# Kernel tuning notes

Measured on AMD Instinct MI355X. Metric: run time of the kernel, lower is better.

## Reference

```python
import jax, jax.numpy as jnp
import numpy as np

T_PRED = 30   # max_pred_time * hz
B = 2048      # number of trajectory segments (batch)
D = 256       # n_hidden_after_deconv
DH = 128      # n_hidden_after_deconv / 2


def setup_inputs() -> dict:
    key = jax.random.key(0)
    k1, k2, k3, k4 = jax.random.split(key, 4)
    return {
        "encode_samples": jax.random.normal(k1, (T_PRED, B, D), dtype=jnp.float32),
        "representation_cur": jax.random.normal(k2, (B, DH), dtype=jnp.float32),
        "Wk_w": jax.random.normal(k3, (T_PRED, D, DH), dtype=jnp.float32) * (1.0 / np.sqrt(DH)),
        "Wk_b": jax.random.normal(k4, (T_PRED, D), dtype=jnp.float32) * 0.01,
    }


def reference(encode_samples, representation_cur, Wk_w, Wk_b):
    # encode_samples: [T, B, D] future encoder outputs (c_{t+i})
    # Wk_w: [T, D, DH] per-step Linear weights (torch layout [out,in]); Wk_b: [T, D]
    T, Bn, Dd = encode_samples.shape
    # pred[i] = Wk[i](representation_cur)  -> [T, B, D]
    pred = jnp.einsum('bh,tdh->tbd', representation_cur, Wk_w) + Wk_b[:, None, :]
    # total_i = encode_samples[i] @ pred[i].T  -> [T, B, B]
    totals = jnp.einsum('tbd,tcd->tbc', encode_samples, pred)
    # nce += sum(diag(log_softmax(total, dim=1))) per step (torch LogSoftmax default dim=1 on 2D)
    logp = jax.nn.log_softmax(totals, axis=2)
    nce = jnp.sum(jnp.diagonal(logp, axis1=1, axis2=2))
    calc_step = Bn * T  # all pred_steps > T-1 (all segments long enough)
    nce = nce / (-1.0 * calc_step)
    # accuracy from the LAST step (matches the original loop-carried `correct`/`batch_idx`)
    probs = jax.nn.softmax(totals[-1], axis=1)          # softmax over dim=1
    correct = jnp.sum(jnp.argmax(probs, axis=0) == jnp.arange(Bn))  # argmax over dim=0
    accuracy = correct.astype(jnp.float32) / Bn
    return (accuracy, nce, jnp.asarray(Bn), jnp.asarray(calc_step))
```

## Files before the change

### kernel.cpp

```cpp
#include <hip/hip_runtime.h>
#include <math.h>

typedef unsigned short u16;
typedef unsigned int   u32;
typedef unsigned long long u64;

#define T_PRED 30
#define BN 2048
#define DD 256
#define DHH 128
#define ESHIFT 64.0f

typedef __attribute__((ext_vector_type(8))) short short8;
typedef __attribute__((ext_vector_type(4))) float f32x4;

#define WS_S      4096
#define WS_TABLE  (WS_S + 245760)
#define WS_ZEND   (WS_TABLE + 16384)
#define WS_WH     WS_ZEND
#define WS_WL     (WS_WH + 1966080)
#define WS_RH     (WS_WL + 1966080)
#define WS_RL     (WS_RH + 524288)
#define WS_GH     (WS_RL + 524288)
#define WS_GL29   (WS_GH + 15728640)
#define WS_T29    (WS_GL29 + 524288)

__device__ __forceinline__ u16 bf16_rne(float f) {
    u32 u = __float_as_uint(f);
    u32 r = u + 0x7fffu + ((u >> 16) & 1u);
    return (u16)(r >> 16);
}

__device__ __forceinline__ short8 pack_hi8(const float* f) {
    short8 r;
#pragma unroll
    for (int k = 0; k < 8; ++k) r[k] = (short)(u16)(__float_as_uint(f[k]) >> 16);
    return r;
}
__device__ __forceinline__ short8 pack_lo8(const float* f) {
    short8 r;
#pragma unroll
    for (int k = 0; k < 8; ++k) {
        float hf = __uint_as_float(__float_as_uint(f[k]) & 0xffff0000u);
        r[k] = (short)bf16_rne(f[k] - hf);
    }
    return r;
}

#define AS1 __attribute__((address_space(1)))
#define AS3 __attribute__((address_space(3)))

__global__ __launch_bounds__(256) void prep_kernel(
    const float* __restrict__ rep, const float* __restrict__ Ww,
    u16* __restrict__ Rh, u16* __restrict__ Rl,
    u16* __restrict__ Wh, u16* __restrict__ Wl, u32* __restrict__ wsz)
{
    const int bx = blockIdx.x, tid = threadIdx.x;
    for (int i = bx * 256 + tid; i < 66560; i += 32768) wsz[i] = 0;

    if (bx < 120) {
        __shared__ float tile[64][132];
        const int t = bx >> 2, d0 = (bx & 3) * 64;
        for (int it = 0; it < 8; ++it) {
            int idx = tid + it * 256;
            int row = idx >> 5, off = (idx & 31) * 4;
            *(float4*)&tile[row][off] =
                *(const float4*)&Ww[((size_t)t * DD + d0 + row) * DHH + off];
        }
        __syncthreads();
        const int h = tid >> 1, half = tid & 1;
        const bool lo = (t == T_PRED - 1);
        for (int d4 = 0; d4 < 32; d4 += 4) {
            ushort4 hv, lv;
            u16* hp = (u16*)&hv; u16* lp = (u16*)&lv;
#pragma unroll
            for (int k = 0; k < 4; ++k) {
                float v = tile[half * 32 + d4 + k][h];
                u16 hb = bf16_rne(v);
                hp[k] = hb;
                float hf = __uint_as_float((u32)hb << 16);
                lp[k] = bf16_rne(v - hf);
            }
            size_t o = (size_t)t * DHH * DD + (size_t)h * DD + d0 + half * 32 + d4;
            *(ushort4*)&Wh[o] = hv;
            if (lo) *(ushort4*)&Wl[o] = lv;
        }
    } else {
        int base = (bx - 120) * 256 + tid;
        for (int p = 0; p < 32; ++p) {
            int i = base + p * 2048;
            float4 v = ((const float4*)rep)[i];
            float vv[4] = {v.x, v.y, v.z, v.w};
            u16 h[4], l[4];
#pragma unroll
            for (int k = 0; k < 4; ++k) {
                h[k] = bf16_rne(vv[k]);
                float hf = __uint_as_float((u32)h[k] << 16);
                l[k] = bf16_rne(vv[k] - hf);
            }
            ((ushort4*)Rh)[i] = make_ushort4(h[0], h[1], h[2], h[3]);
            ((ushort4*)Rl)[i] = make_ushort4(l[0], l[1], l[2], l[3]);
        }
    }
}

__global__ __launch_bounds__(256) void g_fused_kernel(
    const float* __restrict__ E, const u16* __restrict__ Wh,
    const u16* __restrict__ Wl, u16* __restrict__ Gh,
    u16* __restrict__ Gh29, u16* __restrict__ Gl29)
{
    __shared__ __attribute__((aligned(16))) u32 esm[2][4096];
    __shared__ __attribute__((aligned(16))) u16 wsm[2][4096];
    const int y    = blockIdx.y;
    const int tid  = threadIdx.x;
    const int lane = tid & 63;
    const int w    = tid >> 6;
    const int ml   = lane & 15;
    const int quad = lane >> 4;

    if (y < 29) {
        const int t    = y;
        const int row0 = blockIdx.x * 128;
        const int wr   = (w >> 1) * 64;
        const int wc   = (w & 1) * 64;
        const float* Et = E + (size_t)t * BN * DD;
        const u16*   Wt = Wh + (size_t)t * DHH * DD;
        const int erow_l = lane >> 3, eunit = lane & 7;
        const int wcol_l = lane >> 2, wunit = lane & 3;

        auto stage = [&](int buf, int kc) {
#pragma unroll
            for (int n = 0; n < 4; ++n) {
                int q = w * 4 + n;
                int row = q * 8 + erow_l;
                int unit = (eunit - row) & 7;
                const float* g = Et + (size_t)(row0 + row) * DD + kc * 32 + unit * 4;
                __builtin_amdgcn_global_load_lds((const AS1 u32*)g,
                    (AS3 u32*)(&esm[buf][q * 256]), 16, 0, 0);
            }
#pragma unroll
            for (int n = 0; n < 2; ++n) {
                int q = w * 2 + n;
                int col = q * 16 + wcol_l;
                int unit = (wunit - col) & 3;
                const u16* g = Wt + (size_t)col * DD + kc * 32 + unit * 8;
                __builtin_amdgcn_global_load_lds((const AS1 u32*)g,
                    (AS3 u32*)(&wsm[buf][q * 512]), 16, 0, 0);
            }
        };

        f32x4 acc[4][4];
#pragma unroll
        for (int i = 0; i < 4; ++i)
#pragma unroll
            for (int j = 0; j < 4; ++j) acc[i][j] = (f32x4){0.f, 0.f, 0.f, 0.f};

        stage(0, 0);
        __syncthreads();
#pragma unroll 1
        for (int kc = 0; kc < 8; ++kc) {
            if (kc < 7) stage((kc + 1) & 1, kc + 1);
            const int pb = kc & 1;
            short8 ah[4], bh[4];
#pragma unroll
            for (int i = 0; i < 4; ++i) {
                int row = wr + i * 16 + ml;
                float4 f0 = *(const float4*)&esm[pb][row * 32 + (((quad * 2 + 0 + row) & 7) * 4)];
                float4 f1 = *(const float4*)&esm[pb][row * 32 + (((quad * 2 + 1 + row) & 7) * 4)];
                float f[8] = {f0.x, f0.y, f0.z, f0.w, f1.x, f1.y, f1.z, f1.w};
                ah[i] = pack_hi8(f);
            }
#pragma unroll
            for (int j = 0; j < 4; ++j) {
                int col = wc + j * 16 + ml;
                bh[j] = *(const short8*)&wsm[pb][col * 32 + ((quad + col) & 3) * 8];
            }
#pragma unroll
            for (int i = 0; i < 4; ++i)
#pragma unroll
                for (int j = 0; j < 4; ++j)
                    acc[i][j] = __builtin_amdgcn_mfma_f32_16x16x32_bf16(ah[i], bh[j], acc[i][j], 0, 0, 0);
            __syncthreads();
        }

#pragma unroll
        for (int i = 0; i < 4; ++i)
#pragma unroll
            for (int j = 0; j < 4; ++j)
#pragma unroll
                for (int r = 0; r < 4; ++r) {
                    int row = row0 + wr + i * 16 + quad * 4 + r;
                    int col = wc + j * 16 + ml;
                    Gh[((size_t)t * BN + row) * DHH + col] = bf16_rne(acc[i][j][r]);
                }
    } else {
        const int row0 = ((y - 29) * 16 + blockIdx.x) * 32;
        const int wc   = w * 32;
        const size_t tE = (size_t)(T_PRED - 1) * BN * DD;
        const size_t tW = (size_t)(T_PRED - 1) * DHH * DD;

#pragma unroll 1
        for (int rr = 0; rr < 32; rr += 16) {
            f32x4 acc[2];
            acc[0] = (f32x4){0.f, 0.f, 0.f, 0.f};
            acc[1] = (f32x4){0.f, 0.f, 0.f, 0.f};
#pragma unroll
            for (int kc = 0; kc < 8; ++kc) {
                const float* ep = E + tE + (size_t)(row0 + rr + ml) * DD + kc * 32 + quad * 8;
                float4 e0 = *(const float4*)ep;
                float4 e1 = *(const float4*)(ep + 4);
                float f[8] = {e0.x, e0.y, e0.z, e0.w, e1.x, e1.y, e1.z, e1.w};
                short8 ah = pack_hi8(f);
                short8 al = pack_lo8(f);
#pragma unroll
                for (int j = 0; j < 2; ++j) {
                    size_t o = tW + (size_t)(wc + j * 16 + ml) * DD + kc * 32 + quad * 8;
                    short8 bh = *(const short8*)(Wh + o);
                    short8 bl = *(const short8*)(Wl + o);
                    acc[j] = __builtin_amdgcn_mfma_f32_16x16x32_bf16(ah, bh, acc[j], 0, 0, 0);
                    acc[j] = __builtin_amdgcn_mfma_f32_16x16x32_bf16(ah, bl, acc[j], 0, 0, 0);
                    acc[j] = __builtin_amdgcn_mfma_f32_16x16x32_bf16(al, bh, acc[j], 0, 0, 0);
                }
            }
#pragma unroll
            for (int j = 0; j < 2; ++j)
#pragma unroll
                for (int r = 0; r < 4; ++r) {
                    int row = row0 + rr + quad * 4 + r;
                    int col = wc + j * 16 + ml;
                    float v = acc[j][r];
                    u16 hb = bf16_rne(v);
                    float hf = __uint_as_float((u32)hb << 16);
                    Gh29[(size_t)row * DHH + col] = hb;
                    Gl29[(size_t)row * DHH + col] = bf16_rne(v - hf);
                }
        }
    }
}

__global__ __launch_bounds__(512, 4) void nce_fused_kernel(
    const u16* __restrict__ Gh, const u16* __restrict__ Gh29,
    const u16* __restrict__ Gl29, const u16* __restrict__ Rh,
    const u16* __restrict__ Rl, float* __restrict__ S,
    float* __restrict__ tot29, float* __restrict__ nce_acc)
{
    __shared__ __attribute__((aligned(16))) u16 sm[32768];
    const int z    = blockIdx.z;
    const int tid  = threadIdx.x;
    const int lane = tid & 63;
    const int w    = tid >> 6;
    const int ml   = lane & 15;
    const int quad = lane >> 4;
    float* S29 = S + (size_t)(T_PRED - 1) * BN;

    if (z < 29) {
        const int t  = z;
        const int c0 = (int)blockIdx.x << 8;
        const int r0 = (int)blockIdx.y << 8;

#pragma unroll
        for (int n = 0; n < 8; ++n) {
            const int q   = (w << 3) + n;
            const int U   = (q << 6) | lane;
            const int col = U >> 4;
            const int g   = ((U & 15) - col) & 15;
            const u16* src = Rh + (size_t)(c0 + col) * DHH + g * 8;
            __builtin_amdgcn_global_load_lds((const AS1 u32*)src,
                (AS3 u32*)(&sm[q << 9]), 16, 0, 0);
        }

        short8 ah[2][4];
#pragma unroll
        for (int i = 0; i < 2; ++i)
#pragma unroll
            for (int kc = 0; kc < 4; ++kc)
                ah[i][kc] = *(const short8*)(Gh +
                    ((size_t)t * BN + r0 + (w << 5) + (i << 4) + ml) * DHH
                    + (kc << 5) + (quad << 3));

        float ssum[2][4];
#pragma unroll
        for (int i = 0; i < 2; ++i)
#pragma unroll
            for (int r = 0; r < 4; ++r) ssum[i][r] = 0.f;
        float dsum = 0.f;
        const bool dblk = (c0 == r0);
        const int rbase = r0 + (w << 5) + (quad << 2);

        __syncthreads();

#pragma unroll 1
        for (int ch = 0; ch < 8; ++ch) {
            f32x4 acc[2][2];
#pragma unroll
            for (int i = 0; i < 2; ++i)
#pragma unroll
                for (int j = 0; j < 2; ++j) acc[i][j] = (f32x4){0.f, 0.f, 0.f, 0.f};

#pragma unroll
            for (int kc = 0; kc < 4; ++kc) {
                const int slot = ((kc << 2) + quad + ml) & 15;
                const short8 bh0 = *(const short8*)&sm[((ch << 5) + ml) * 128 + (slot << 3)];
                const short8 bh1 = *(const short8*)&sm[((ch << 5) + 16 + ml) * 128 + (slot << 3)];
                acc[0][0] = __builtin_amdgcn_mfma_f32_16x16x32_bf16(ah[0][kc], bh0, acc[0][0], 0, 0, 0);
                acc[0][1] = __builtin_amdgcn_mfma_f32_16x16x32_bf16(ah[0][kc], bh1, acc[0][1], 0, 0, 0);
                acc[1][0] = __builtin_amdgcn_mfma_f32_16x16x32_bf16(ah[1][kc], bh0, acc[1][0], 0, 0, 0);
                acc[1][1] = __builtin_amdgcn_mfma_f32_16x16x32_bf16(ah[1][kc], bh1, acc[1][1], 0, 0, 0);
            }

#pragma unroll
            for (int i = 0; i < 2; ++i)
#pragma unroll
                for (int j = 0; j < 2; ++j)
#pragma unroll
                    for (int r = 0; r < 4; ++r) {
                        float v = acc[i][j][r];
                        ssum[i][r] += __expf(v - ESHIFT);
                        if (dblk) {
                            int row = rbase + (i << 4) + r;
                            int col = c0 + (ch << 5) + (j << 4) + ml;
                            if (row == col) dsum += v;
                        }
                    }
        }

#pragma unroll
        for (int i = 0; i < 2; ++i)
#pragma unroll
            for (int r = 0; r < 4; ++r) {
                float v = ssum[i][r];
#pragma unroll
                for (int o = 1; o < 16; o <<= 1) v += __shfl_xor(v, o, 64);
                if (ml == 0)
                    atomicAdd(S + (size_t)t * BN + rbase + (i << 4) + r, v);
            }
        if (dblk) {
            float dv = dsum;
#pragma unroll
            for (int o = 1; o < 64; o <<= 1) dv += __shfl_xor(dv, o, 64);
            if (lane == 0) atomicAdd(nce_acc, -dv);
        }
    } else {
        const int idx = ((z - 29) << 6) + ((int)blockIdx.y << 3) + (int)blockIdx.x;
        const int rb  = idx >> 4, cb = idx & 15;
        const int r0  = rb << 7, c0 = cb << 7;
        const bool dblk = (rb == cb);

#pragma unroll
        for (int n = 0; n < 8; ++n) {
            const int q    = (w << 3) + n;
            const int U    = (q << 6) | lane;
            const int colL = (U >> 4) & 127;
            const int half = U >> 11;
            const int g    = ((U & 15) - colL) & 15;
            const u16* src = (half ? Rl : Rh) + (size_t)(c0 + colL) * DHH + g * 8;
            __builtin_amdgcn_global_load_lds((const AS1 u32*)src,
                (AS3 u32*)(&sm[q << 9]), 16, 0, 0);
        }

        short8 ah[4], al[4];
#pragma unroll
        for (int kc = 0; kc < 4; ++kc) {
            size_t o = (size_t)(r0 + (w << 4) + ml) * DHH + (kc << 5) + (quad << 3);
            ah[kc] = *(const short8*)(Gh29 + o);
            al[kc] = *(const short8*)(Gl29 + o);
        }

        float esum[4];
#pragma unroll
        for (int r = 0; r < 4; ++r) esum[r] = 0.f;
        float dsum = 0.f;
        const int rbase = r0 + (w << 4) + (quad << 2);

        __syncthreads();

#pragma unroll 1
        for (int ch = 0; ch < 4; ++ch) {
            f32x4 acc[2];
            acc[0] = (f32x4){0.f, 0.f, 0.f, 0.f};
            acc[1] = (f32x4){0.f, 0.f, 0.f, 0.f};
#pragma unroll
            for (int kc = 0; kc < 4; ++kc) {
                const int slot = ((kc << 2) + quad + ml) & 15;
                const int i0 = ((ch << 5) + ml) * 128 + (slot << 3);
                const int i1 = i0 + 16 * 128;
                const short8 bh0 = *(const short8*)&sm[i0];
                const short8 bl0 = *(const short8*)&sm[16384 + i0];
                const short8 bh1 = *(const short8*)&sm[i1];
                const short8 bl1 = *(const short8*)&sm[16384 + i1];
                acc[0] = __builtin_amdgcn_mfma_f32_16x16x32_bf16(ah[kc], bh0, acc[0], 0, 0, 0);
                acc[0] = __builtin_amdgcn_mfma_f32_16x16x32_bf16(ah[kc], bl0, acc[0], 0, 0, 0);
                acc[0] = __builtin_amdgcn_mfma_f32_16x16x32_bf16(al[kc], bh0, acc[0], 0, 0, 0);
                acc[1] = __builtin_amdgcn_mfma_f32_16x16x32_bf16(ah[kc], bh1, acc[1], 0, 0, 0);
                acc[1] = __builtin_amdgcn_mfma_f32_16x16x32_bf16(ah[kc], bl1, acc[1], 0, 0, 0);
                acc[1] = __builtin_amdgcn_mfma_f32_16x16x32_bf16(al[kc], bh1, acc[1], 0, 0, 0);
            }

#pragma unroll
            for (int j = 0; j < 2; ++j)
#pragma unroll
                for (int r = 0; r < 4; ++r) {
                    float v = acc[j][r];
                    int row = rbase + r;
                    int col = c0 + (ch << 5) + (j << 4) + ml;
                    tot29[(size_t)row * BN + col] = v;
                    esum[r] += __expf(v - ESHIFT);
                    if (dblk && row == col) dsum += v;
                }
        }

#pragma unroll
        for (int r = 0; r < 4; ++r) {
            float v = esum[r];
#pragma unroll
            for (int o = 1; o < 16; o <<= 1) v += __shfl_xor(v, o, 64);
            if (ml == 0) atomicAdd(S29 + rbase + r, v);
        }
        if (dblk) {
            float dv = dsum;
#pragma unroll
            for (int o = 1; o < 64; o <<= 1) dv += __shfl_xor(dv, o, 64);
            if (lane == 0) atomicAdd(nce_acc, -dv);
        }
    }
}

__device__ __forceinline__ u32 fenc(float f) {
    u32 u = __float_as_uint(f);
    return (u & 0x80000000u) ? ~u : (u | 0x80000000u);
}

__global__ __launch_bounds__(256) void argmax_fin_kernel(
    const float* __restrict__ tot29, const float* __restrict__ S,
    u64* __restrict__ table, u32* __restrict__ done,
    float* __restrict__ nce_acc, float* __restrict__ out)
{
    __shared__ float lse_s[128];
    __shared__ float part[4];
    __shared__ u32 lastflag;
    __shared__ int cpart[4];
    const int tid = threadIdx.x;
    const int c   = blockIdx.x * 256 + tid;
    const int b0  = blockIdx.y * 128;
    const float* S29 = S + (size_t)(T_PRED - 1) * BN;

    {
        const int base = ((int)blockIdx.y * 8 + (int)blockIdx.x) * 480;
        float v = 0.f;
        for (int i = tid; i < 480; i += 256)
            v += ESHIFT + __logf(S[base + i]);
#pragma unroll
        for (int o = 1; o < 64; o <<= 1) v += __shfl_xor(v, o, 64);
        if ((tid & 63) == 0) part[tid >> 6] = v;
        __syncthreads();
        if (tid == 0)
            atomicAdd(nce_acc, part[0] + part[1] + part[2] + part[3]);
    }

    if (tid < 128) lse_s[tid] = ESHIFT + __logf(S29[b0 + tid]);
    __syncthreads();

    float best = -3.4e38f; int bi = 0;
    for (int b = 0; b < 128; ++b) {
        float v = tot29[(size_t)(b0 + b) * BN + c] - lse_s[b];
        if (v > best) { best = v; bi = b0 + b; }
    }
    u64 key = ((u64)fenc(best) << 32) | (u32)(0xFFFFFFFFu - (u32)bi);
    atomicMax(table + c, key);

    __threadfence();
    if (tid == 0) lastflag = (atomicAdd(done, 1u) == 127u);
    __syncthreads();
    if (!lastflag) return;

    int cnt = 0;
    for (int i = tid; i < BN; i += 256) {
        u64 k = atomicAdd(table + i, 0ull);
        u32 b = 0xFFFFFFFFu - (u32)(k & 0xFFFFFFFFull);
        if ((int)b == i) cnt++;
    }
#pragma unroll
    for (int o = 1; o < 64; o <<= 1) cnt += __shfl_xor(cnt, o, 64);
    if ((tid & 63) == 0) cpart[tid >> 6] = cnt;
    __syncthreads();
    if (tid == 0) {
        int correct = cpart[0] + cpart[1] + cpart[2] + cpart[3];
        float nce = atomicAdd(nce_acc, 0.0f);
        out[0] = (float)correct / (float)BN;
        out[1] = nce / (float)(BN * T_PRED);
        out[2] = (float)BN;
        out[3] = (float)(BN * T_PRED);
    }
}

extern "C" void kernel_launch(void* const* d_in, const int* in_sizes, int n_in,
                              void* d_out, int out_size, void* d_ws, size_t ws_size,
                              hipStream_t stream) {
    const float* E   = (const float*)d_in[0];
    const float* rep = (const float*)d_in[1];
    const float* Ww  = (const float*)d_in[2];
    float* out = (float*)d_out;

    char* ws = (char*)d_ws;
    float* nce_acc = (float*)(ws + 0);
    u32*   done    = (u32*)(ws + 8);
    float* S       = (float*)(ws + WS_S);
    u64*   table   = (u64*)(ws + WS_TABLE);
    u16*   Wh      = (u16*)(ws + WS_WH);
    u16*   Wl      = (u16*)(ws + WS_WL);
    u16*   Rh      = (u16*)(ws + WS_RH);
    u16*   Rl      = (u16*)(ws + WS_RL);
    u16*   Gh      = (u16*)(ws + WS_GH);
    u16*   Gh29    = Gh + (size_t)(T_PRED - 1) * BN * DHH;
    u16*   Gl29    = (u16*)(ws + WS_GL29);
    float* tot29   = (float*)(ws + WS_T29);

    prep_kernel<<<dim3(128), 256, 0, stream>>>(rep, Ww, Rh, Rl, Wh, Wl, (u32*)ws);
    g_fused_kernel<<<dim3(16, 33), 256, 0, stream>>>(E, Wh, Wl, Gh, Gh29, Gl29);
    nce_fused_kernel<<<dim3(8, 8, 33), 512, 0, stream>>>(Gh, Gh29, Gl29, Rh, Rl,
                                                         S, tot29, nce_acc);
    argmax_fin_kernel<<<dim3(8, 16), 256, 0, stream>>>(tot29, S, table, done,
                                                       nce_acc, out);
}
```

Measured before the change: 189.2 us.

## Preload full per-step W tile into LDS and stream E rows directly to registers

The G-projection kernel now loads the whole 128x256 bf16 weight slice for a step into LDS once per block (with rotated swizzle) instead of double-buffering E and W chunks across the K loop. Each of 8 waves handles 16 rows of E loaded straight from global into registers and computes all 128 output columns, removing the per-chunk barriers. The special last step is folded into the same 16x30 grid with 512 threads, using the same LDS W-high tile and global W-low loads for its three-term split product. This trades E reuse across waves via LDS for fewer syncs and less staging, and it lowers parallelism for the last step from 64 blocks to 16.

```diff
diff --git a/kernel.cpp b/kernel.cpp
--- a/kernel.cpp
+++ b/kernel.cpp
@@ -104,13 +104,12 @@
     }
 }
 
-__global__ __launch_bounds__(256) void g_fused_kernel(
+__global__ __launch_bounds__(512) void g_fused_kernel(
     const float* __restrict__ E, const u16* __restrict__ Wh,
     const u16* __restrict__ Wl, u16* __restrict__ Gh,
     u16* __restrict__ Gh29, u16* __restrict__ Gl29)
 {
-    __shared__ __attribute__((aligned(16))) u32 esm[2][4096];
-    __shared__ __attribute__((aligned(16))) u16 wsm[2][4096];
+    __shared__ __attribute__((aligned(16))) u16 wsm[32768];
     const int y    = blockIdx.y;
     const int tid  = threadIdx.x;
     const int lane = tid & 63;
@@ -118,123 +117,92 @@
     const int ml   = lane & 15;
     const int quad = lane >> 4;
 
+    const int t    = (y < 29) ? y : 29;
+    const u16* Wt  = Wh + (size_t)t * DHH * DD;
+
+#pragma unroll
+    for (int n = 0; n < 8; ++n) {
+        const int q = (w << 3) + n;
+        const int U = (q << 6) | lane;
+        const int c = U >> 5;
+        const int g = ((U & 31) - c) & 31;
+        const u16* src = Wt + (size_t)c * DD + g * 8;
+        __builtin_amdgcn_global_load_lds((const AS1 u32*)src,
+            (AS3 u32*)(&wsm[q << 9]), 16, 0, 0);
+    }
+
+    const int row0 = (int)blockIdx.x << 7;
+    const int erow = row0 + (w << 4) + ml;
+    const float* ebase = E + ((size_t)t * BN + erow) * DD;
+    const int orow = row0 + (w << 4) + (quad << 2);
+
     if (y < 29) {
-        const int t    = y;
-        const int row0 = blockIdx.x * 128;
-        const int wr   = (w >> 1) * 64;
-        const int wc   = (w & 1) * 64;
-        const float* Et = E + (size_t)t * BN * DD;
-        const u16*   Wt = Wh + (size_t)t * DHH * DD;
-        const int erow_l = lane >> 3, eunit = lane & 7;
-        const int wcol_l = lane >> 2, wunit = lane & 3;
-
-        auto stage = [&](int buf, int kc) {
-#pragma unroll
-            for (int n = 0; n < 4; ++n) {
-                int q = w * 4 + n;
-                int row = q * 8 + erow_l;
-                int unit = (eunit - row) & 7;
-                const float* g = Et + (size_t)(row0 + row) * DD + kc * 32 + unit * 4;
-                __builtin_amdgcn_global_load_lds((const AS1 u32*)g,
-                    (AS3 u32*)(&esm[buf][q * 256]), 16, 0, 0);
-            }
-#pragma unroll
-            for (int n = 0; n < 2; ++n) {
-                int q = w * 2 + n;
-                int col = q * 16 + wcol_l;
-                int unit = (wunit - col) & 3;
-                const u16* g = Wt + (size_t)col * DD + kc * 32 + unit * 8;
-                __builtin_amdgcn_global_load_lds((const AS1 u32*)g,
-                    (AS3 u32*)(&wsm[buf][q * 512]), 16, 0, 0);
-            }
-        };
-
-        f32x4 acc[4][4];
-#pragma unroll
-        for (int i = 0; i < 4; ++i)
-#pragma unroll
-            for (int j = 0; j < 4; ++j) acc[i][j] = (f32x4){0.f, 0.f, 0.f, 0.f};
-
-        stage(0, 0);
-        __syncthreads();
-#pragma unroll 1
+        f32x4 acc[8];
+#pragma unroll
+        for (int j = 0; j < 8; ++j) acc[j] = (f32x4){0.f, 0.f, 0.f, 0.f};
+
+        __syncthreads();
+
+#pragma unroll
         for (int kc = 0; kc < 8; ++kc) {
-            if (kc < 7) stage((kc + 1) & 1, kc + 1);
-            const int pb = kc & 1;
-            short8 ah[4], bh[4];
-#pragma unroll
-            for (int i = 0; i < 4; ++i) {
-                int row = wr + i * 16 + ml;
-                float4 f0 = *(const float4*)&esm[pb][row * 32 + (((quad * 2 + 0 + row) & 7) * 4)];
-                float4 f1 = *(const float4*)&esm[pb][row * 32 + (((quad * 2 + 1 + row) & 7) * 4)];
-                float f[8] = {f0.x, f0.y, f0.z, f0.w, f1.x, f1.y, f1.z, f1.w};
-                ah[i] = pack_hi8(f);
-            }
-#pragma unroll
-            for (int j = 0; j < 4; ++j) {
-                int col = wc + j * 16 + ml;
-                bh[j] = *(const short8*)&wsm[pb][col * 32 + ((quad + col) & 3) * 8];
-            }
-#pragma unroll
-            for (int i = 0; i < 4; ++i)
-#pragma unroll
-                for (int j = 0; j < 4; ++j)
-                    acc[i][j] = __builtin_amdgcn_mfma_f32_16x16x32_bf16(ah[i], bh[j], acc[i][j], 0, 0, 0);
-            __syncthreads();
-        }
-
-#pragma unroll
-        for (int i = 0; i < 4; ++i)
-#pragma unroll
-            for (int j = 0; j < 4; ++j)
-#pragma unroll
-                for (int r = 0; r < 4; ++r) {
-                    int row = row0 + wr + i * 16 + quad * 4 + r;
-                    int col = wc + j * 16 + ml;
-                    Gh[((size_t)t * BN + row) * DHH + col] = bf16_rne(acc[i][j][r]);
-                }
+            float4 e0 = *(const float4*)(ebase + (kc << 5) + (quad << 3));
+            float4 e1 = *(const float4*)(ebase + (kc << 5) + (quad << 3) + 4);
+            float f[8] = {e0.x, e0.y, e0.z, e0.w, e1.x, e1.y, e1.z, e1.w};
+            short8 ah = pack_hi8(f);
+#pragma unroll
+            for (int j = 0; j < 8; ++j) {
+                const int h    = (j << 4) + ml;
+                const int slot = (((kc << 2) + quad + h) & 31);
+                const short8 bh = *(const short8*)&wsm[(h << 8) + (slot << 3)];
+                acc[j] = __builtin_amdgcn_mfma_f32_16x16x32_bf16(ah, bh, acc[j], 0, 0, 0);
+            }
+        }
+
+#pragma unroll
+        for (int j = 0; j < 8; ++j)
+#pragma unroll
+            for (int r = 0; r < 4; ++r)
+                Gh[((size_t)t * BN + orow + r) * DHH + (j << 4) + ml] =
+                    bf16_rne(acc[j][r]);
     } else {
-        const int row0 = ((y - 29) * 16 + blockIdx.x) * 32;
-        const int wc   = w * 32;
-        const size_t tE = (size_t)(T_PRED - 1) * BN * DD;
-        const size_t tW = (size_t)(T_PRED - 1) * DHH * DD;
-
-#pragma unroll 1
-        for (int rr = 0; rr < 32; rr += 16) {
-            f32x4 acc[2];
-            acc[0] = (f32x4){0.f, 0.f, 0.f, 0.f};
-            acc[1] = (f32x4){0.f, 0.f, 0.f, 0.f};
-#pragma unroll
-            for (int kc = 0; kc < 8; ++kc) {
-                const float* ep = E + tE + (size_t)(row0 + rr + ml) * DD + kc * 32 + quad * 8;
-                float4 e0 = *(const float4*)ep;
-                float4 e1 = *(const float4*)(ep + 4);
-                float f[8] = {e0.x, e0.y, e0.z, e0.w, e1.x, e1.y, e1.z, e1.w};
-                short8 ah = pack_hi8(f);
-                short8 al = pack_lo8(f);
-#pragma unroll
-                for (int j = 0; j < 2; ++j) {
-                    size_t o = tW + (size_t)(wc + j * 16 + ml) * DD + kc * 32 + quad * 8;
-                    short8 bh = *(const short8*)(Wh + o);
-                    short8 bl = *(const short8*)(Wl + o);
-                    acc[j] = __builtin_amdgcn_mfma_f32_16x16x32_bf16(ah, bh, acc[j], 0, 0, 0);
-                    acc[j] = __builtin_amdgcn_mfma_f32_16x16x32_bf16(ah, bl, acc[j], 0, 0, 0);
-                    acc[j] = __builtin_amdgcn_mfma_f32_16x16x32_bf16(al, bh, acc[j], 0, 0, 0);
-                }
-            }
-#pragma unroll
-            for (int j = 0; j < 2; ++j)
-#pragma unroll
-                for (int r = 0; r < 4; ++r) {
-                    int row = row0 + rr + quad * 4 + r;
-                    int col = wc + j * 16 + ml;
-                    float v = acc[j][r];
-                    u16 hb = bf16_rne(v);
-                    float hf = __uint_as_float((u32)hb << 16);
-                    Gh29[(size_t)row * DHH + col] = hb;
-                    Gl29[(size_t)row * DHH + col] = bf16_rne(v - hf);
-                }
-        }
+        const u16* Wlt = Wl + (size_t)(T_PRED - 1) * DHH * DD;
+        f32x4 acc[8];
+#pragma unroll
+        for (int j = 0; j < 8; ++j) acc[j] = (f32x4){0.f, 0.f, 0.f, 0.f};
+
+        __syncthreads();
+
+#pragma unroll
+        for (int kc = 0; kc < 8; ++kc) {
+            float4 e0 = *(const float4*)(ebase + (kc << 5) + (quad << 3));
+            float4 e1 = *(const float4*)(ebase + (kc << 5) + (quad << 3) + 4);
+            float f[8] = {e0.x, e0.y, e0.z, e0.w, e1.x, e1.y, e1.z, e1.w};
+            short8 ah = pack_hi8(f);
+            short8 al = pack_lo8(f);
+#pragma unroll
+            for (int j = 0; j < 8; ++j) {
+                const int h    = (j << 4) + ml;
+                const int slot = (((kc << 2) + quad + h) & 31);
+                const short8 bh = *(const short8*)&wsm[(h << 8) + (slot << 3)];
+                const short8 bl = *(const short8*)(Wlt + (size_t)h * DD
+                                                   + (kc << 5) + (quad << 3));
+                acc[j] = __builtin_amdgcn_mfma_f32_16x16x32_bf16(ah, bh, acc[j], 0, 0, 0);
+                acc[j] = __builtin_amdgcn_mfma_f32_16x16x32_bf16(ah, bl, acc[j], 0, 0, 0);
+                acc[j] = __builtin_amdgcn_mfma_f32_16x16x32_bf16(al, bh, acc[j], 0, 0, 0);
+            }
+        }
+
+#pragma unroll
+        for (int j = 0; j < 8; ++j)
+#pragma unroll
+            for (int r = 0; r < 4; ++r) {
+                float v = acc[j][r];
+                u16 hb = bf16_rne(v);
+                float hf = __uint_as_float((u32)hb << 16);
+                size_t o = (size_t)(orow + r) * DHH + (j << 4) + ml;
+                Gh29[o] = hb;
+                Gl29[o] = bf16_rne(v - hf);
+            }
     }
 }
 
@@ -516,7 +484,7 @@
     float* tot29   = (float*)(ws + WS_T29);
 
     prep_kernel<<<dim3(128), 256, 0, stream>>>(rep, Ww, Rh, Rl, Wh, Wl, (u32*)ws);
-    g_fused_kernel<<<dim3(16, 33), 256, 0, stream>>>(E, Wh, Wl, Gh, Gh29, Gl29);
+    g_fused_kernel<<<dim3(16, 30), 512, 0, stream>>>(E, Wh, Wl, Gh, Gh29, Gl29);
     nce_fused_kernel<<<dim3(8, 8, 33), 512, 0, stream>>>(Gh, Gh29, Gl29, Rh, Rl,
                                                          S, tot29, nce_acc);
     argmax_fin_kernel<<<dim3(8, 16), 256, 0, stream>>>(tot29, S, table, done,
```

New measurement: 200.5 us. 1.06x slower.
